# Kernel optimization log

Measured on AMD Instinct MI355X. Metric: run time of the kernel, lower is better.

The kernel has to match this reference:

```python
import jax, jax.numpy as jnp
import numpy as np

B, S, D = 2, 2048, 3584
H, KV, HD = 28, 4, 128
N_REP = H // KV          # 7
MAX_S = 2048
SCALE = HD ** -0.5
ROPE_BASE = 1_000_000.0  # Qwen2 rope theta


def _rope_tables(max_s, hd, base):
    inv = 1.0 / (base ** (np.arange(0, hd, 2, dtype=np.float32) / hd))  # [hd/2]
    ang = np.arange(max_s, dtype=np.float32)[:, None] * inv[None, :]    # [S, hd/2]
    return jnp.asarray(np.cos(ang)), jnp.asarray(np.sin(ang))


def apply_rotary(x, cos, sin):
    # x: [b, s, h, hd] with interleaved complex pairs (torch view_as_complex layout)
    xr = x[..., 0::2]
    xi = x[..., 1::2]
    cos = cos[None, :, None, :]
    sin = sin[None, :, None, :]
    yr = xr * cos - xi * sin
    yi = xr * sin + xi * cos
    return jnp.stack([yr, yi], axis=-1).reshape(x.shape)


def setup_inputs() -> dict:
    key = jax.random.key(0)
    ks = jax.random.split(key, 8)
    w = 0.02
    x = jax.random.normal(ks[0], (B, S, D), jnp.float32)
    wq_w = jax.random.normal(ks[1], (H * HD, D), jnp.float32) * w
    wq_b = jax.random.normal(ks[2], (H * HD,), jnp.float32) * w
    wk_w = jax.random.normal(ks[3], (KV * HD, D), jnp.float32) * w
    wk_b = jax.random.normal(ks[4], (KV * HD,), jnp.float32) * w
    wv_w = jax.random.normal(ks[5], (KV * HD, D), jnp.float32) * w
    wv_b = jax.random.normal(ks[6], (KV * HD,), jnp.float32) * w
    wo_w = jax.random.normal(ks[7], (D, H * HD), jnp.float32) * w
    k_cache = jnp.zeros((B, MAX_S, KV, HD), jnp.float32)
    v_cache = jnp.zeros((B, MAX_S, KV, HD), jnp.float32)
    freqs_cos, freqs_sin = _rope_tables(MAX_S, HD, ROPE_BASE)
    # causal additive mask [s, t]; large-negative instead of -inf for safe grads
    mask = jnp.triu(jnp.full((S, S), -1e9, jnp.float32), k=1)
    return {"x": x, "wq_w": wq_w, "wq_b": wq_b, "wk_w": wk_w, "wk_b": wk_b,
            "wv_w": wv_w, "wv_b": wv_b, "wo_w": wo_w,
            "k_cache": k_cache, "v_cache": v_cache,
            "freqs_cos": freqs_cos, "freqs_sin": freqs_sin,
            "mask": mask, "start_pos": 0}


def reference(x, wq_w, wq_b, wk_w, wk_b, wv_w, wv_b, wo_w,
              k_cache, v_cache, freqs_cos, freqs_sin, mask, start_pos):
    bsz, seqlen, _ = x.shape
    end_pos = start_pos + seqlen
    q = (x @ wq_w.T + wq_b).reshape(bsz, seqlen, H, HD)
    k = (x @ wk_w.T + wk_b).reshape(bsz, seqlen, KV, HD)
    v = (x @ wv_w.T + wv_b).reshape(bsz, seqlen, KV, HD)
    cos = jax.lax.dynamic_slice_in_dim(freqs_cos, start_pos, seqlen, 0)
    sin = jax.lax.dynamic_slice_in_dim(freqs_sin, start_pos, seqlen, 0)
    q = apply_rotary(q, cos, sin)
    k = apply_rotary(k, cos, sin)
    # KV-cache write
    k_cache = jax.lax.dynamic_update_slice(k_cache, k, (0, start_pos, 0, 0))
    v_cache = jax.lax.dynamic_update_slice(v_cache, v, (0, start_pos, 0, 0))
    keys = k_cache[:bsz, :end_pos]    # [b, t, kv, hd]
    values = v_cache[:bsz, :end_pos]
    # GQA: repeat_interleave kv heads to n_heads
    keys = jnp.repeat(keys, N_REP, axis=2)      # [b, t, h, hd]
    values = jnp.repeat(values, N_REP, axis=2)
    scores = jnp.einsum('bshd,bthd->bsht', q, keys) * SCALE
    scores = scores + mask[None, :, None, :]
    probs = jax.nn.softmax(scores.astype(jnp.float32), axis=-1).astype(x.dtype)
    out = jnp.einsum('bsht,bthd->bshd', probs, values)
    out = out.reshape(bsz, seqlen, H * HD)
    return out @ wo_w.T
```

## Files before the change

### kernel.cpp

```cpp
#include <hip/hip_runtime.h>
#include <hip/hip_bf16.h>

typedef __attribute__((ext_vector_type(4)))  float  f32x4;
typedef __attribute__((ext_vector_type(16))) float  f32x16;
typedef __attribute__((ext_vector_type(8)))  __bf16 bf16x8;
typedef __attribute__((ext_vector_type(4)))  __bf16 bf16x4;
typedef __attribute__((ext_vector_type(4)))  unsigned int u32x4;

constexpr int S_LEN = 2048, DMODEL = 3584, NH = 28, NKV = 4, HD = 128, NREP = 7;
constexpr float SCALE_LOG2 = 0.1275174331f;

__device__ __forceinline__ unsigned int pack2(float a, float b) {
  unsigned short ua = __builtin_bit_cast(unsigned short, (__bf16)a);
  unsigned short ub = __builtin_bit_cast(unsigned short, (__bf16)b);
  return (unsigned int)ua | ((unsigned int)ub << 16);
}

__global__ void cvt_kernel(const float* __restrict__ in, __bf16* __restrict__ out, int n4) {
  int i = blockIdx.x * blockDim.x + threadIdx.x;
  if (i >= n4) return;
  float4 v = reinterpret_cast<const float4*>(in)[i];
  bf16x4 o;
  o[0] = (__bf16)v.x; o[1] = (__bf16)v.y; o[2] = (__bf16)v.z; o[3] = (__bf16)v.w;
  reinterpret_cast<bf16x4*>(out)[i] = o;
}

__global__ void zero_ctr_kernel(int* p) { *p = 0; }

#define GLDS16(gsrc, ldst)                                                              \
  __builtin_amdgcn_global_load_lds((const __attribute__((address_space(1))) void*)(gsrc),\
                                   (__attribute__((address_space(3))) void*)(ldst), 16, 0, 0)

template <int MODE>
__global__ __launch_bounds__(512, 2) void gemm256(
    const __bf16* __restrict__ A, const __bf16* __restrict__ Bw,
    const float* __restrict__ bias, void* __restrict__ Cout,
    int M, int N, int K,
    const float* __restrict__ fcos, const float* __restrict__ fsin,
    const int* __restrict__ sp_ptr, float scale)
{
  extern __shared__ char smem[];
  const int tid = threadIdx.x;
  const int lane = tid & 63, wid = tid >> 6;
  const int wm = wid >> 2, wn = wid & 3;
  const int l15 = lane & 15, g = (lane >> 4) & 3;

  const int chunk = gridDim.x >> 3;
  const int wg = (blockIdx.x & 7) * chunk + (blockIdx.x >> 3);
  const int nbx = N >> 8;
  const int by = wg / nbx, bx = wg % nbx;
  const int row0 = by * 256, col0 = bx * 256;

  const int srL   = 16 * (tid >> 6) + ((tid >> 2) & 15);
  const int cperm = ((tid & 3) * 8) ^ (((tid >> 5) & 1) * 16);
  const __bf16* pA0 = A + (size_t)(row0 + srL) * K + cperm;
  const __bf16* pA1 = pA0 + (size_t)128 * K;
  const __bf16* pB0 = Bw + (size_t)(col0 + srL) * K + cperm;
  const __bf16* pB1 = pB0 + (size_t)128 * K;
  char* ldsA = smem + tid * 16;
  char* ldsB = smem + 65536 + tid * 16;

  const int sw = ((l15 >> 3) & 1) << 5;
  const int aoff = wm * 8192 + l15 * 64 + ((g * 16) ^ sw);
  const int boff = 65536 + wn * 4096 + l15 * 64 + ((g * 16) ^ sw);

  f32x4 acc[8][4] = {};
  const int nt = K >> 5;

#pragma unroll
  for (int pt = 0; pt < 3; pt++) {
    const size_t ko = (size_t)pt * 32;
    char* sA = ldsA + pt * 16384;
    char* sB = ldsB + pt * 16384;
    GLDS16(pA0 + ko, sA);
    GLDS16(pA1 + ko, sA + 8192);
    GLDS16(pB0 + ko, sB);
    GLDS16(pB1 + ko, sB + 8192);
  }
  asm volatile("s_waitcnt vmcnt(8)" ::: "memory");
  __builtin_amdgcn_s_barrier();
  __builtin_amdgcn_sched_barrier(0);

  for (int t = 0; t < nt; t++) {
    const int slot = (t & 3) * 16384;
    const char* sa = smem + slot + aoff;
    const char* sb = smem + slot + boff;
    bf16x8 af[4], bfv[4];

#pragma unroll
    for (int fm = 0; fm < 4; fm++)
      af[fm] = *reinterpret_cast<const bf16x8*>(sa + fm * 1024);
#pragma unroll
    for (int fn = 0; fn < 4; fn++)
      bfv[fn] = *reinterpret_cast<const bf16x8*>(sb + fn * 1024);
    if (t + 3 < nt) {
      const size_t ko = (size_t)(t + 3) * 32;
      char* sA = ldsA + ((t + 3) & 3) * 16384;
      GLDS16(pA0 + ko, sA);
      GLDS16(pA1 + ko, sA + 8192);
    }
    asm volatile("s_waitcnt lgkmcnt(0)" ::: "memory");
    __builtin_amdgcn_sched_barrier(0);
    __builtin_amdgcn_s_setprio(1);
#pragma unroll
    for (int fn = 0; fn < 4; fn++)
#pragma unroll
      for (int fm = 0; fm < 4; fm++)
        acc[fm][fn] = __builtin_amdgcn_mfma_f32_16x16x32_bf16(af[fm], bfv[fn], acc[fm][fn], 0, 0, 0);
    __builtin_amdgcn_s_setprio(0);
    __builtin_amdgcn_s_barrier();
    __builtin_amdgcn_sched_barrier(0);

#pragma unroll
    for (int fm = 0; fm < 4; fm++)
      af[fm] = *reinterpret_cast<const bf16x8*>(sa + (4 + fm) * 1024);
    if (t + 3 < nt) {
      const size_t ko = (size_t)(t + 3) * 32;
      char* sB = ldsB + ((t + 3) & 3) * 16384;
      GLDS16(pB0 + ko, sB);
      GLDS16(pB1 + ko, sB + 8192);
    }
    asm volatile("s_waitcnt lgkmcnt(0)" ::: "memory");
    __builtin_amdgcn_sched_barrier(0);
    __builtin_amdgcn_s_setprio(1);
#pragma unroll
    for (int fn = 0; fn < 4; fn++)
#pragma unroll
      for (int fm = 0; fm < 4; fm++)
        acc[4 + fm][fn] = __builtin_amdgcn_mfma_f32_16x16x32_bf16(af[fm], bfv[fn], acc[4 + fm][fn], 0, 0, 0);
    __builtin_amdgcn_s_setprio(0);

    if (t < nt - 3)       asm volatile("s_waitcnt vmcnt(8)" ::: "memory");
    else if (t == nt - 3) asm volatile("s_waitcnt vmcnt(4)" ::: "memory");
    else if (t == nt - 2) asm volatile("s_waitcnt vmcnt(0)" ::: "memory");
    __builtin_amdgcn_s_barrier();
    __builtin_amdgcn_sched_barrier(0);
  }

  if constexpr (MODE == 0) {
    float* C = (float*)Cout;
#pragma unroll
    for (int fm = 0; fm < 8; fm++) {
      const int row = row0 + wm * 128 + fm * 16 + 4 * g;
#pragma unroll
      for (int fn = 0; fn < 4; fn++) {
        const int col = col0 + wn * 64 + fn * 16 + l15;
#pragma unroll
        for (int r = 0; r < 4; r++)
          C[(size_t)(row + r) * N + col] = acc[fm][fn][r];
      }
    }
  } else {
    __bf16* C = (__bf16*)Cout;
    const int sp = sp_ptr[0];
    float bval[4];
#pragma unroll
    for (int fn = 0; fn < 4; fn++) bval[fn] = bias[col0 + wn * 64 + fn * 16 + l15];
#pragma unroll
    for (int fm = 0; fm < 8; fm++) {
#pragma unroll
      for (int fn = 0; fn < 4; fn++) {
        const int col = col0 + wn * 64 + fn * 16 + l15;
        const int i = (col & (HD - 1)) >> 1;
#pragma unroll
        for (int r = 0; r < 4; r++) {
          const int row = row0 + wm * 128 + fm * 16 + 4 * g + r;
          float y = acc[fm][fn][r] + bval[fn];
          float p = __shfl_xor(y, 1);
          const int spos = sp + (row & (S_LEN - 1));
          const float c = fcos[spos * (HD / 2) + i];
          const float sn = fsin[spos * (HD / 2) + i];
          y = (col & 1) ? (p * sn + y * c) : (y * c - p * sn);
          C[(size_t)row * N + col] = (__bf16)(y * scale);
        }
      }
    }
  }
}

__global__ __launch_bounds__(256) void gemm_kv(
    const __bf16* __restrict__ A,
    const __bf16* __restrict__ Wk, const float* __restrict__ bk, __bf16* __restrict__ Ko,
    const __bf16* __restrict__ Wv, const float* __restrict__ bv, __bf16* __restrict__ Vo,
    const float* __restrict__ fcos, const float* __restrict__ fsin,
    const int* __restrict__ sp_ptr)
{
  constexpr int N = 512, K = 3584;
  __shared__ __bf16 As[128 * 32];
  __shared__ __bf16 Bs[128 * 32];
  const int tid = threadIdx.x;
  const int lane = tid & 63, wid = tid >> 6;
  const int l15 = lane & 15, g = lane >> 4;
  const int wr = wid >> 1, wc = wid & 1;
  const bool isK = blockIdx.x < 4;
  const __bf16* Bw = isK ? Wk : Wv;
  const float* bias = isK ? bk : bv;
  __bf16* Cout = isK ? Ko : Vo;
  const int row0 = blockIdx.y * 128;
  const int col0 = (blockIdx.x & 3) * 128;

  f32x4 acc[4][4] = {};

  const int srow = tid >> 2;
  const int scol = (tid & 3) * 8;
  const __bf16* Ag0 = A + (size_t)(row0 + srow) * K + scol;
  const __bf16* Ag1 = Ag0 + (size_t)64 * K;
  const __bf16* Bg0 = Bw + (size_t)(col0 + srow) * K + scol;
  const __bf16* Bg1 = Bg0 + (size_t)64 * K;
  __bf16* As0 = As + tid * 8;
  __bf16* As1 = As + 2048 + tid * 8;
  __bf16* Bs0 = Bs + tid * 8;
  __bf16* Bs1 = Bs + 2048 + tid * 8;

  for (int k0 = 0; k0 < K; k0 += 32) {
    GLDS16(Ag0 + k0, As0);
    GLDS16(Ag1 + k0, As1);
    GLDS16(Bg0 + k0, Bs0);
    GLDS16(Bg1 + k0, Bs1);
    __syncthreads();
    bf16x8 af[4], bfr[4];
#pragma unroll
    for (int m = 0; m < 4; m++)
      af[m] = *reinterpret_cast<const bf16x8*>(As + (wr * 64 + m * 16 + l15) * 32 + g * 8);
#pragma unroll
    for (int n = 0; n < 4; n++)
      bfr[n] = *reinterpret_cast<const bf16x8*>(Bs + (wc * 64 + n * 16 + l15) * 32 + g * 8);
#pragma unroll
    for (int m = 0; m < 4; m++)
#pragma unroll
      for (int n = 0; n < 4; n++)
        acc[m][n] = __builtin_amdgcn_mfma_f32_16x16x32_bf16(af[m], bfr[n], acc[m][n], 0, 0, 0);
    __syncthreads();
  }

  const int sp = sp_ptr[0];
#pragma unroll
  for (int m = 0; m < 4; m++) {
#pragma unroll
    for (int n = 0; n < 4; n++) {
      const int col = col0 + wc * 64 + n * 16 + l15;
      const float bval = bias[col];
      f32x4 v = acc[m][n];
#pragma unroll
      for (int r = 0; r < 4; r++) {
        const int row = row0 + wr * 64 + m * 16 + 4 * g + r;
        float y = v[r] + bval;
        if (isK) {
          float p = __shfl_xor(y, 1);
          const int i = (col & (HD - 1)) >> 1;
          const int spos = sp + (row & (S_LEN - 1));
          const float c = fcos[spos * (HD / 2) + i];
          const float sn = fsin[spos * (HD / 2) + i];
          y = (col & 1) ? (p * sn + y * c) : (y * c - p * sn);
        }
        Cout[(size_t)row * N + col] = (__bf16)y;
      }
    }
  }
}

__global__ void vtrans_kernel(const __bf16* __restrict__ Vg, __bf16* __restrict__ Vt) {
  __shared__ __bf16 t[32][33];
  const int bkv = blockIdx.z;
  const int b = bkv >> 2, kv = bkv & 3;
  const int s0 = blockIdx.x * 32, h0 = blockIdx.y * 32;
  const int tid = threadIdx.x;
#pragma unroll
  for (int c = 0; c < 4; c++) {
    int idx = c * 256 + tid;
    int sr = idx >> 5, hc = idx & 31;
    t[sr][hc] = Vg[(((size_t)b * S_LEN + s0 + sr) * NKV + kv) * HD + h0 + hc];
  }
  __syncthreads();
#pragma unroll
  for (int c = 0; c < 4; c++) {
    int idx = c * 256 + tid;
    int hr = idx >> 5, sc = idx & 31;
    Vt[(((size_t)b * NKV + kv) * HD + h0 + hr) * S_LEN + s0 + sc] = t[sc][hr];
  }
}

__global__ __launch_bounds__(256, 2) void attn_kernel(
    const __bf16* __restrict__ Qb, const __bf16* __restrict__ Kb,
    const __bf16* __restrict__ Vt, __bf16* __restrict__ Ob, int* __restrict__ ctr)
{
  __shared__ __align__(16) char asmem[65536];
  __shared__ int jsh;

  const int tid = threadIdx.x, lane = tid & 63, wid = tid >> 6;
  const int l31 = lane & 31, hh = lane >> 5;

  const int trow = tid >> 4;
  const int kcol = (((tid & 15) * 16) ^ ((trow & 7) << 4)) >> 1;
  const int vrow = tid >> 3;
  const int vcol = (((tid & 7) * 16) ^ ((vrow & 7) << 4)) >> 1;

  constexpr int NITEMS = 16 * NH * 2;

  while (true) {
    if (tid == 0) jsh = atomicAdd(ctr, 1);
    __syncthreads();
    const int j = jsh;
    if (j >= NITEMS) break;

    const int qi = 15 - (j / 56);
    const int r56 = j % 56;
    const int h = r56 >> 1, b = r56 & 1;
    const int kvh = h / NREP;
    const int qw = qi * 128 + wid * 32;
    const int qg = qw + l31;

    const __bf16* Kbase = Kb + ((size_t)b * S_LEN * NKV + kvh) * HD;
    const __bf16* Vbase = Vt + ((size_t)b * NKV + kvh) * (size_t)HD * S_LEN;

    bf16x8 qf[8];
    {
      const __bf16* qp = Qb + (((size_t)b * S_LEN + qg) * NH + h) * HD + hh * 8;
#pragma unroll
      for (int c = 0; c < 8; c++) qf[c] = *reinterpret_cast<const bf16x8*>(qp + c * 16);
    }

    f32x16 o[4] = {};
    float mrun = -3.0e38f, lsum = 0.0f;

    const int ntiles = 2 * qi + 2;

#define STAGE(T, S)                                                                     \
    do {                                                                                \
      const int k0_ = (T) * 64;                                                         \
      char* Kd_ = asmem + (S) * 32768;                                                  \
      char* Vd_ = Kd_ + 16384;                                                          \
      _Pragma("unroll")                                                                 \
      for (int p = 0; p < 4; p++) {                                                     \
        GLDS16(Kbase + (size_t)(k0_ + p * 16 + trow) * (NKV * HD) + kcol,               \
               Kd_ + (p * 256 + tid) * 16);                                             \
        GLDS16(Vbase + (size_t)(p * 32 + vrow) * S_LEN + k0_ + vcol,                    \
               Vd_ + (p * 256 + tid) * 16);                                             \
      }                                                                                 \
    } while (0)

    STAGE(0, 0);

    for (int t = 0; t < ntiles; t++) {
      __syncthreads();
      if (t + 1 < ntiles) STAGE(t + 1, (t + 1) & 1);

      const char* Ksb = asmem + (t & 1) * 32768;
      const char* Vsb = Ksb + 16384;
      const int k0 = t * 64;

      f32x16 s0 = {}, s1 = {};
      {
        const char* kp0 = Ksb + l31 * 256;
        const char* kp1 = kp0 + 32 * 256;
        const int sw = (l31 & 7) << 4;
        __builtin_amdgcn_s_setprio(1);
#pragma unroll
        for (int c = 0; c < 8; c++) {
          const int cb = (c * 32 + hh * 16) ^ sw;
          bf16x8 kf0 = *reinterpret_cast<const bf16x8*>(kp0 + cb);
          s0 = __builtin_amdgcn_mfma_f32_32x32x16_bf16(kf0, qf[c], s0, 0, 0, 0);
          bf16x8 kf1 = *reinterpret_cast<const bf16x8*>(kp1 + cb);
          s1 = __builtin_amdgcn_mfma_f32_32x32x16_bf16(kf1, qf[c], s1, 0, 0, 0);
        }
        __builtin_amdgcn_s_setprio(0);
      }

      if (k0 + 63 > qw) {
#pragma unroll
        for (int r = 0; r < 16; r++) {
          const int kvo = k0 + ((r & 3) + 8 * (r >> 2)) + 4 * hh;
          if (kvo > qg)      s0[r] = -1.0e9f;
          if (kvo + 32 > qg) s1[r] = -1.0e9f;
        }
      }

      float pmax = -3.0e38f;
#pragma unroll
      for (int r = 0; r < 16; r++) { pmax = fmaxf(pmax, s0[r]); pmax = fmaxf(pmax, s1[r]); }
      pmax = fmaxf(pmax, __shfl_xor(pmax, 32));
      if (!__all(pmax <= mrun + 11.5f)) {
        const float mnew = fmaxf(mrun, pmax);
        const float fs = exp2f(mrun - mnew);
        lsum *= fs;
#pragma unroll
        for (int dt = 0; dt < 4; dt++) o[dt] *= fs;
        mrun = mnew;
      }
      float psum = 0.0f;
#pragma unroll
      for (int r = 0; r < 16; r++) {
        s0[r] = exp2f(s0[r] - mrun); psum += s0[r];
        s1[r] = exp2f(s1[r] - mrun); psum += s1[r];
      }
      lsum += psum;

      unsigned int pk[2][8], px[2][8];
#pragma unroll
      for (int jj = 0; jj < 8; jj++) {
        pk[0][jj] = pack2(s0[2 * jj], s0[2 * jj + 1]);
        pk[1][jj] = pack2(s1[2 * jj], s1[2 * jj + 1]);
      }
#pragma unroll
      for (int tt = 0; tt < 2; tt++)
#pragma unroll
        for (int jj = 0; jj < 8; jj++) px[tt][jj] = __shfl_xor(pk[tt][jj], 32);

      __builtin_amdgcn_s_setprio(1);
#pragma unroll
      for (int tt = 0; tt < 2; tt++) {
#pragma unroll
        for (int c2 = 0; c2 < 2; c2++) {
          u32x4 pb4;
          if (hh == 0)
            pb4 = (u32x4){pk[tt][4 * c2], pk[tt][4 * c2 + 1], px[tt][4 * c2], px[tt][4 * c2 + 1]};
          else
            pb4 = (u32x4){px[tt][4 * c2 + 2], px[tt][4 * c2 + 3], pk[tt][4 * c2 + 2], pk[tt][4 * c2 + 3]};
          bf16x8 pbf = __builtin_bit_cast(bf16x8, pb4);
          const int colb = tt * 64 + c2 * 32 + hh * 16;
#pragma unroll
          for (int dt = 0; dt < 4; dt++) {
            const int d = dt * 32 + l31;
            bf16x8 vf = *reinterpret_cast<const bf16x8*>(Vsb + d * 128 + (colb ^ ((d & 7) << 4)));
            o[dt] = __builtin_amdgcn_mfma_f32_32x32x16_bf16(vf, pbf, o[dt], 0, 0, 0);
          }
        }
      }
      __builtin_amdgcn_s_setprio(0);
    }
#undef STAGE

    lsum += __shfl_xor(lsum, 32);
    const float inv = 1.0f / lsum;
    char* my = asmem + wid * 8192;
#pragma unroll
    for (int dt = 0; dt < 4; dt++) {
#pragma unroll
      for (int jj = 0; jj < 8; jj++) {
        const int r = 2 * jj;
        const int d = dt * 32 + ((r & 3) + 8 * (r >> 2)) + 4 * hh;
        const unsigned int w = pack2(o[dt][r] * inv, o[dt][r + 1] * inv);
        *reinterpret_cast<unsigned int*>(my + ((l31 * 256 + d * 2) ^ ((l31 & 7) << 4))) = w;
      }
    }
#pragma unroll
    for (int jj = 0; jj < 8; jj++) {
      const int idx = jj * 64 + lane;
      const int row = idx >> 4, c16 = idx & 15;
      u32x4 val = *reinterpret_cast<u32x4*>(my + row * 256 + ((c16 * 16) ^ ((row & 7) << 4)));
      *reinterpret_cast<u32x4*>(Ob + (size_t)(b * S_LEN + qw + row) * (NH * HD) + h * HD + c16 * 8) = val;
    }
  }
}

extern "C" void kernel_launch(void* const* d_in, const int* in_sizes, int n_in,
                              void* d_out, int out_size, void* d_ws, size_t ws_size,
                              hipStream_t stream) {
  (void)in_sizes; (void)n_in; (void)out_size; (void)ws_size;
  const float* x    = (const float*)d_in[0];
  const float* wq_w = (const float*)d_in[1];
  const float* wq_b = (const float*)d_in[2];
  const float* wk_w = (const float*)d_in[3];
  const float* wk_b = (const float*)d_in[4];
  const float* wv_w = (const float*)d_in[5];
  const float* wv_b = (const float*)d_in[6];
  const float* wo_w = (const float*)d_in[7];
  const float* fcos = (const float*)d_in[10];
  const float* fsin = (const float*)d_in[11];
  const int*   spp  = (const int*)d_in[13];
  float* out = (float*)d_out;

  constexpr size_t XB_N = (size_t)4096 * 3584;
  constexpr size_t WQ_N = (size_t)3584 * 3584;
  constexpr size_t WK_N = (size_t)512 * 3584;
  constexpr size_t WO_N = (size_t)3584 * 3584;
  constexpr size_t KB_N = (size_t)4096 * 512;

  __bf16* xb  = (__bf16*)d_ws;
  __bf16* wqb = xb + XB_N;
  __bf16* wkb = wqb + WQ_N;
  __bf16* wvb = wkb + WK_N;
  __bf16* wob = wvb + WK_N;
  __bf16* Qb  = wob + WO_N;
  __bf16* Kb  = Qb + XB_N;
  __bf16* Vg  = Kb + KB_N;
  __bf16* Vt  = Vg + KB_N;
  int*    ctr = (int*)(Vt + KB_N);
  __bf16* Ob  = xb;

  auto cvt = [&](const float* src, __bf16* dst, size_t n) {
    int n4 = (int)(n / 4);
    cvt_kernel<<<(n4 + 255) / 256, 256, 0, stream>>>(src, dst, n4);
  };
  cvt(x, xb, XB_N);
  cvt(wq_w, wqb, WQ_N);
  cvt(wk_w, wkb, WK_N);
  cvt(wv_w, wvb, WK_N);
  cvt(wo_w, wob, WO_N);
  zero_ctr_kernel<<<1, 1, 0, stream>>>(ctr);

  gemm256<2><<<dim3(224), 512, 131072, stream>>>(xb, wqb, wq_b, Qb, 4096, 3584, 3584,
                                                 fcos, fsin, spp, SCALE_LOG2);
  gemm_kv<<<dim3(8, 32), 256, 0, stream>>>(xb, wkb, wk_b, Kb, wvb, wv_b, Vg,
                                           fcos, fsin, spp);
  vtrans_kernel<<<dim3(64, 4, 8), 256, 0, stream>>>(Vg, Vt);
  attn_kernel<<<dim3(512), 256, 0, stream>>>(Qb, Kb, Vt, Ob, ctr);
  gemm256<0><<<dim3(224), 512, 131072, stream>>>(Ob, wob, nullptr, out, 4096, 3584, 3584,
                                                 nullptr, nullptr, nullptr, 1.0f);
}
```

Baseline: 450.8 us.

## Fuse fp32-to-bf16 conversions into one launch and merge GEMM k-step halves

Replaces five separate conversion launches and the counter-zeroing launch with a single grid-stride kernel that converts all five tensors and zeroes the counter. Inside the 256x256 GEMM main loop, all A and B fragments for a k-step are now loaded up front. The A and B prefetches are issued together, and the mid-iteration barrier is dropped, with a partial lgkmcnt wait letting the first MFMA half start early. This cuts launch overhead and one barrier per iteration, at the cost of more live fragment registers, which could pressure occupancy under launch_bounds(512,2).

Measured after the change: 432.9 us. 1.04x faster.

```diff
diff --git a/kernel.cpp b/kernel.cpp
--- a/kernel.cpp
+++ b/kernel.cpp
@@ -16,16 +16,33 @@
   return (unsigned int)ua | ((unsigned int)ub << 16);
 }
 
-__global__ void cvt_kernel(const float* __restrict__ in, __bf16* __restrict__ out, int n4) {
-  int i = blockIdx.x * blockDim.x + threadIdx.x;
-  if (i >= n4) return;
-  float4 v = reinterpret_cast<const float4*>(in)[i];
-  bf16x4 o;
-  o[0] = (__bf16)v.x; o[1] = (__bf16)v.y; o[2] = (__bf16)v.z; o[3] = (__bf16)v.w;
-  reinterpret_cast<bf16x4*>(out)[i] = o;
-}
-
-__global__ void zero_ctr_kernel(int* p) { *p = 0; }
+__global__ void cvt5_kernel(const float* __restrict__ s0, const float* __restrict__ s1,
+                            const float* __restrict__ s2, const float* __restrict__ s3,
+                            const float* __restrict__ s4,
+                            __bf16* __restrict__ d0, __bf16* __restrict__ d1,
+                            __bf16* __restrict__ d2, __bf16* __restrict__ d3,
+                            __bf16* __restrict__ d4,
+                            int n0, int n1, int n2, int n3, int* __restrict__ ctr, int total) {
+  if (blockIdx.x == 0 && threadIdx.x == 0) *ctr = 0;
+  for (int i = blockIdx.x * blockDim.x + threadIdx.x; i < total; i += gridDim.x * blockDim.x) {
+    const float* s; __bf16* d; int j = i;
+    if (j < n0) { s = s0; d = d0; }
+    else { j -= n0;
+      if (j < n1) { s = s1; d = d1; }
+      else { j -= n1;
+        if (j < n2) { s = s2; d = d2; }
+        else { j -= n2;
+          if (j < n3) { s = s3; d = d3; }
+          else { j -= n3; s = s4; d = d4; }
+        }
+      }
+    }
+    float4 v = reinterpret_cast<const float4*>(s)[j];
+    bf16x4 o;
+    o[0] = (__bf16)v.x; o[1] = (__bf16)v.y; o[2] = (__bf16)v.z; o[3] = (__bf16)v.w;
+    reinterpret_cast<bf16x4*>(d)[j] = o;
+  }
+}
 
 #define GLDS16(gsrc, ldst)                                                              \
   __builtin_amdgcn_global_load_lds((const __attribute__((address_space(1))) void*)(gsrc),\
@@ -85,20 +102,38 @@
     const int slot = (t & 3) * 16384;
     const char* sa = smem + slot + aoff;
     const char* sb = smem + slot + boff;
-    bf16x8 af[4], bfv[4];
-
-#pragma unroll
-    for (int fm = 0; fm < 4; fm++)
-      af[fm] = *reinterpret_cast<const bf16x8*>(sa + fm * 1024);
+    bf16x8 a0[4], a1[4], bfv[4];
+
 #pragma unroll
     for (int fn = 0; fn < 4; fn++)
       bfv[fn] = *reinterpret_cast<const bf16x8*>(sb + fn * 1024);
+#pragma unroll
+    for (int fm = 0; fm < 4; fm++)
+      a0[fm] = *reinterpret_cast<const bf16x8*>(sa + fm * 1024);
+#pragma unroll
+    for (int fm = 0; fm < 4; fm++)
+      a1[fm] = *reinterpret_cast<const bf16x8*>(sa + (4 + fm) * 1024);
+
     if (t + 3 < nt) {
       const size_t ko = (size_t)(t + 3) * 32;
       char* sA = ldsA + ((t + 3) & 3) * 16384;
+      char* sB = ldsB + ((t + 3) & 3) * 16384;
       GLDS16(pA0 + ko, sA);
       GLDS16(pA1 + ko, sA + 8192);
-    }
+      GLDS16(pB0 + ko, sB);
+      GLDS16(pB1 + ko, sB + 8192);
+    }
+
+    asm volatile("s_waitcnt lgkmcnt(4)" ::: "memory");
+    __builtin_amdgcn_sched_barrier(0);
+    __builtin_amdgcn_s_setprio(1);
+#pragma unroll
+    for (int fn = 0; fn < 4; fn++)
+#pragma unroll
+      for (int fm = 0; fm < 4; fm++)
+        acc[fm][fn] = __builtin_amdgcn_mfma_f32_16x16x32_bf16(a0[fm], bfv[fn], acc[fm][fn], 0, 0, 0);
+    __builtin_amdgcn_s_setprio(0);
+
     asm volatile("s_waitcnt lgkmcnt(0)" ::: "memory");
     __builtin_amdgcn_sched_barrier(0);
     __builtin_amdgcn_s_setprio(1);
@@ -106,28 +141,7 @@
     for (int fn = 0; fn < 4; fn++)
 #pragma unroll
       for (int fm = 0; fm < 4; fm++)
-        acc[fm][fn] = __builtin_amdgcn_mfma_f32_16x16x32_bf16(af[fm], bfv[fn], acc[fm][fn], 0, 0, 0);
-    __builtin_amdgcn_s_setprio(0);
-    __builtin_amdgcn_s_barrier();
-    __builtin_amdgcn_sched_barrier(0);
-
-#pragma unroll
-    for (int fm = 0; fm < 4; fm++)
-      af[fm] = *reinterpret_cast<const bf16x8*>(sa + (4 + fm) * 1024);
-    if (t + 3 < nt) {
-      const size_t ko = (size_t)(t + 3) * 32;
-      char* sB = ldsB + ((t + 3) & 3) * 16384;
-      GLDS16(pB0 + ko, sB);
-      GLDS16(pB1 + ko, sB + 8192);
-    }
-    asm volatile("s_waitcnt lgkmcnt(0)" ::: "memory");
-    __builtin_amdgcn_sched_barrier(0);
-    __builtin_amdgcn_s_setprio(1);
-#pragma unroll
-    for (int fn = 0; fn < 4; fn++)
-#pragma unroll
-      for (int fm = 0; fm < 4; fm++)
-        acc[4 + fm][fn] = __builtin_amdgcn_mfma_f32_16x16x32_bf16(af[fm], bfv[fn], acc[4 + fm][fn], 0, 0, 0);
+        acc[4 + fm][fn] = __builtin_amdgcn_mfma_f32_16x16x32_bf16(a1[fm], bfv[fn], acc[4 + fm][fn], 0, 0, 0);
     __builtin_amdgcn_s_setprio(0);
 
     if (t < nt - 3)       asm volatile("s_waitcnt vmcnt(8)" ::: "memory");
@@ -488,16 +502,12 @@
   int*    ctr = (int*)(Vt + KB_N);
   __bf16* Ob  = xb;
 
-  auto cvt = [&](const float* src, __bf16* dst, size_t n) {
-    int n4 = (int)(n / 4);
-    cvt_kernel<<<(n4 + 255) / 256, 256, 0, stream>>>(src, dst, n4);
-  };
-  cvt(x, xb, XB_N);
-  cvt(wq_w, wqb, WQ_N);
-  cvt(wk_w, wkb, WK_N);
-  cvt(wv_w, wvb, WK_N);
-  cvt(wo_w, wob, WO_N);
-  zero_ctr_kernel<<<1, 1, 0, stream>>>(ctr);
+  constexpr int N0 = (int)(XB_N / 4), N1 = (int)(WQ_N / 4), N2 = (int)(WK_N / 4),
+                N3 = (int)(WK_N / 4), N4 = (int)(WO_N / 4);
+  constexpr int NTOT = N0 + N1 + N2 + N3 + N4;
+  cvt5_kernel<<<2048, 256, 0, stream>>>(x, wq_w, wk_w, wv_w, wo_w,
+                                        xb, wqb, wkb, wvb, wob,
+                                        N0, N1, N2, N3, ctr, NTOT);
 
   gemm256<2><<<dim3(224), 512, 131072, stream>>>(xb, wqb, wq_b, Qb, 4096, 3584, 3584,
                                                  fcos, fsin, spp, SCALE_LOG2);
```
